# Performance work log

Hardware: AMD Instinct MI355X
Metric: run time of the kernel (lower is better)

## Reference

```python
import jax, jax.numpy as jnp
import numpy as np

TEMPERATURE = 0.6
TOP_K = 50
TOP_P = 0.9
REP_PENALTY = 1.2
BATCH, VOCAB, HIST = 256, 128000, 200


def setup_inputs() -> dict:
    key = jax.random.key(0)
    k1, k2 = jax.random.split(key)
    logits = jax.random.normal(k1, (BATCH, VOCAB), dtype=jnp.float32)
    prev_tokens = jax.random.randint(k2, (BATCH, HIST), 0, VOCAB)
    return {"logits": logits, "prev_tokens": prev_tokens}


def reference(logits, prev_tokens):
    B = logits.shape[0]
    rows = jnp.arange(B)[:, None]  # [B,1] row index for scatter

    # --- repetition penalty: mult if <0 else div, on previously seen tokens ---
    vals = jnp.take_along_axis(logits, prev_tokens, axis=1)  # [B,H]
    penalized = jnp.where(vals < 0, vals * REP_PENALTY, vals / REP_PENALTY)
    logits = logits.at[rows, prev_tokens].set(penalized)

    # --- temperature ---
    logits = logits / TEMPERATURE

    # --- top-k filter: mask everything below the k-th largest logit ---
    kth = jax.lax.top_k(logits, TOP_K)[0][:, -1:]  # [B,1]
    logits = jnp.where(logits < kth, -jnp.inf, logits)

    # --- top-p (nucleus) filter: sort desc, cumsum probs, keep prefix <= p ---
    order = jnp.argsort(-logits, axis=-1)                      # [B,V] desc order
    sorted_logits = jnp.take_along_axis(logits, order, axis=-1)
    cum_probs = jnp.cumsum(jax.nn.softmax(sorted_logits, axis=-1), axis=-1)
    remove_sorted = cum_probs > TOP_P
    # shift right so the first token exceeding p is kept (HF semantics)
    remove_sorted = jnp.concatenate(
        [jnp.zeros_like(remove_sorted[:, :1]), remove_sorted[:, :-1]], axis=-1)
    # scatter mask back to vocab order
    remove = jnp.zeros_like(remove_sorted).at[rows, order].set(remove_sorted)
    logits = jnp.where(remove, -jnp.inf, logits)

    # --- distribution parameter of Multinomial(total_count=compare_sample) ---
    probs = jax.nn.softmax(logits, axis=-1)
    return probs
```

## Files before the change

### kernel.cpp

```cpp
#include <hip/hip_runtime.h>
#include <stdint.h>

#define BATCH    256
#define VOCAB    128000
#define HIST     200
#define TOPK     50
#define CAP      2048
#define NTHREADS 1024
#define BITWORDS (VOCAB / 32)

__device__ __forceinline__ unsigned fkey_of(float f) {
  unsigned u = __float_as_uint(f);
  return (u & 0x80000000u) ? ~u : (u | 0x80000000u);
}
__device__ __forceinline__ float f_of_key(unsigned k) {
  unsigned u = (k & 0x80000000u) ? (k & 0x7FFFFFFFu) : ~k;
  return __uint_as_float(u);
}

__global__ __launch_bounds__(NTHREADS) void sample_head_kernel(
    const float* __restrict__ logits, const int* __restrict__ prev,
    float* __restrict__ out)
{
  __shared__ unsigned bitmask[BITWORDS];
  __shared__ unsigned long long keys[CAP];
  __shared__ float evals[CAP];
  __shared__ int s_count;
  __shared__ int s_m, s_j;
  __shared__ float s_maxx, s_Z2;

  const int b   = blockIdx.x;
  const int tid = threadIdx.x;
  const float* row  = logits + (size_t)b * VOCAB;
  float*       orow = out    + (size_t)b * VOCAB;

  for (int i = tid; i < BITWORDS; i += NTHREADS) bitmask[i] = 0u;
  __syncthreads();
  for (int i = tid; i < HIST; i += NTHREADS) {
    int t = prev[b * HIST + i];
    atomicOr(&bitmask[t >> 5], 1u << (t & 31));
  }
  __syncthreads();

  float T = 3.0f;
  float Tlo = 0.f, Thi = 0.f;
  bool hasLo = false, hasHi = false;
  int cnt = 0;

  const float4* row4  = (const float4*)row;
  float4*       orow4 = (float4*)orow;
  const int N4 = VOCAB / 4;

  for (int attempt = 0; attempt < 40; ++attempt) {
    __syncthreads();
    if (tid == 0) s_count = 0;
    __syncthreads();

    for (int i = tid; i < N4; i += NTHREADS) {
      float4 v4 = row4[i];
      if (attempt == 0) orow4[i] = make_float4(0.f, 0.f, 0.f, 0.f);
      int v0 = i * 4;
      unsigned w  = bitmask[v0 >> 5];
      unsigned sh = v0 & 31;
      float vv[4] = {v4.x, v4.y, v4.z, v4.w};
      #pragma unroll
      for (int l = 0; l < 4; ++l) {
        float v = vv[l];
        float y = v;
        if ((w >> (sh + l)) & 1u)
          y = (v < 0.0f) ? v * 1.2f : v / 1.2f;
        if (y > T) {
          float x = y / 0.6f;
          int pos = atomicAdd(&s_count, 1);
          if (pos < CAP) {
            unsigned k = fkey_of(x);
            keys[pos] = ((unsigned long long)k << 32) |
                        (unsigned)(~(unsigned)(v0 + l));
          }
        }
      }
    }
    __syncthreads();
    cnt = s_count;
    if (cnt >= TOPK && cnt <= CAP) break;
    if (cnt < TOPK) { Thi = T; hasHi = true; T = hasLo ? 0.5f * (T + Tlo) : T - 1.0f; }
    else            { Tlo = T; hasLo = true; T = hasHi ? 0.5f * (T + Thi) : T + 1.0f; }
  }
  if (cnt > CAP) cnt = CAP;

  int n = 64;
  while (n < cnt) n <<= 1;
  for (int i = cnt + tid; i < n; i += NTHREADS) keys[i] = 0ull;
  __syncthreads();
  for (int k = 2; k <= n; k <<= 1) {
    for (int j = k >> 1; j > 0; j >>= 1) {
      for (int i = tid; i < n; i += NTHREADS) {
        int l = i ^ j;
        if (l > i) {
          unsigned long long a = keys[i], c = keys[l];
          bool up = (i & k) == 0;
          if (up ? (a < c) : (a > c)) { keys[i] = c; keys[l] = a; }
        }
      }
      __syncthreads();
    }
  }

  if (tid == 0) {
    int kk = (cnt < TOPK) ? cnt : TOPK;
    unsigned kth = (unsigned)(keys[kk - 1] >> 32);
    int m = kk;
    while (m < cnt && (unsigned)(keys[m] >> 32) == kth) m++;
    s_m = m;
    s_maxx = f_of_key((unsigned)(keys[0] >> 32));
  }
  __syncthreads();
  int m = s_m;
  float maxx = s_maxx;
  for (int i = tid; i < m; i += NTHREADS)
    evals[i] = expf(f_of_key((unsigned)(keys[i] >> 32)) - maxx);
  __syncthreads();

  if (tid == 0) {
    float Z = 0.f;
    for (int i = 0; i < m; ++i) Z += evals[i];
    float cum = 0.f;
    int j = 0;
    for (int i = 0; i < m; ++i) {
      if (i > 0 && cum > 0.9f) break;
      cum += evals[i] / Z;
      j = i + 1;
    }
    float Z2 = 0.f;
    for (int i = 0; i < j; ++i) Z2 += evals[i];
    s_j = j; s_Z2 = Z2;
  }
  __syncthreads();

  int j = s_j;
  float Z2 = s_Z2;
  for (int i = tid; i < j; i += NTHREADS) {
    int idx = (int)(~(unsigned)(keys[i] & 0xFFFFFFFFull));
    orow[idx] = evals[i] / Z2;
  }
}

extern "C" void kernel_launch(void* const* d_in, const int* in_sizes, int n_in,
                              void* d_out, int out_size, void* d_ws, size_t ws_size,
                              hipStream_t stream) {
  const float* logits = (const float*)d_in[0];
  const int*   prev   = (const int*)d_in[1];
  float*       out    = (float*)d_out;
  hipLaunchKernelGGL(sample_head_kernel, dim3(BATCH), dim3(NTHREADS), 0, stream,
                     logits, prev, out);
}
```

Measured before the change: 249.1 us.

## Split into multi-block streaming collect kernel and per-row select kernel

New measurement: 258.1 us. +3.6%, slower.

```diff
diff --git a/kernel.cpp b/kernel.cpp
--- a/kernel.cpp
+++ b/kernel.cpp
@@ -5,9 +5,18 @@
 #define VOCAB    128000
 #define HIST     200
 #define TOPK     50
+#define BITWORDS (VOCAB / 32)
+
+#define SLICES   8
+#define NT1      256
+#define NT2      256
+#define LCAP     1024
+#define TRAW     3.0f
+
 #define CAP      2048
 #define NTHREADS 1024
-#define BITWORDS (VOCAB / 32)
+
+typedef float f32x4_t __attribute__((ext_vector_type(4)));
 
 __device__ __forceinline__ unsigned fkey_of(float f) {
   unsigned u = __float_as_uint(f);
@@ -16,6 +25,172 @@
 __device__ __forceinline__ float f_of_key(unsigned k) {
   unsigned u = (k & 0x80000000u) ? (k & 0x7FFFFFFFu) : ~k;
   return __uint_as_float(u);
+}
+
+__global__ __launch_bounds__(NT1) void stream_collect_kernel(
+    const float* __restrict__ logits, float* __restrict__ out,
+    int* __restrict__ cnt_g, uint2* __restrict__ cand_g)
+{
+  const int bid = blockIdx.x;
+  const int b = bid >> 3;
+  const int s = bid & (SLICES - 1);
+  const float4* row4  = (const float4*)(logits + (size_t)b * VOCAB);
+  float4*       orow4 = (float4*)(out + (size_t)b * VOCAB);
+  const int per = (VOCAB / 4) / SLICES;
+  const int lo = s * per, hi = lo + per;
+  int*   cnt  = cnt_g + b;
+  uint2* cand = cand_g + (size_t)b * LCAP;
+
+  const f32x4_t z4 = (f32x4_t)0.f;
+  for (int i = lo + threadIdx.x; i < hi; i += NT1) {
+    float4 v = row4[i];
+    __builtin_nontemporal_store(z4, (f32x4_t*)&orow4[i]);
+    unsigned v0 = 4u * (unsigned)i;
+    if (v.x > TRAW) { int p = atomicAdd(cnt, 1); if (p < LCAP) cand[p] = make_uint2(__float_as_uint(v.x), v0 + 0u); }
+    if (v.y > TRAW) { int p = atomicAdd(cnt, 1); if (p < LCAP) cand[p] = make_uint2(__float_as_uint(v.y), v0 + 1u); }
+    if (v.z > TRAW) { int p = atomicAdd(cnt, 1); if (p < LCAP) cand[p] = make_uint2(__float_as_uint(v.z), v0 + 2u); }
+    if (v.w > TRAW) { int p = atomicAdd(cnt, 1); if (p < LCAP) cand[p] = make_uint2(__float_as_uint(v.w), v0 + 3u); }
+  }
+}
+
+__global__ __launch_bounds__(NT2) void select_kernel(
+    const float* __restrict__ logits, const int* __restrict__ prev,
+    float* __restrict__ out, const int* __restrict__ cnt_g,
+    const uint2* __restrict__ cand_g)
+{
+  __shared__ unsigned bitmask[BITWORDS];
+  __shared__ unsigned long long keys[LCAP];
+  __shared__ float evals[LCAP];
+  __shared__ int s_cnt, s_good, s_m, s_j;
+  __shared__ float s_maxx, s_Z2;
+
+  const int b   = blockIdx.x;
+  const int tid = threadIdx.x;
+  const float* row  = logits + (size_t)b * VOCAB;
+  float*       orow = out    + (size_t)b * VOCAB;
+
+  for (int i = tid; i < BITWORDS; i += NT2) bitmask[i] = 0u;
+  if (tid == 0) s_good = 0;
+  __syncthreads();
+  for (int i = tid; i < HIST; i += NT2) {
+    int t = prev[b * HIST + i];
+    atomicOr(&bitmask[t >> 5], 1u << (t & 31));
+  }
+  __syncthreads();
+
+  int cnt = cnt_g[b];
+  int mn = cnt < LCAP ? cnt : LCAP;
+  const uint2* cand = cand_g + (size_t)b * LCAP;
+  for (int i = tid; i < mn; i += NT2) {
+    uint2 c = cand[i];
+    float v = __uint_as_float(c.x);
+    unsigned idx = c.y;
+    float y = v;
+    if ((bitmask[idx >> 5] >> (idx & 31)) & 1u)
+      y = (v < 0.0f) ? v * 1.2f : v / 1.2f;
+    float x = y / 0.6f;
+    keys[i] = ((unsigned long long)fkey_of(x) << 32) |
+              (unsigned)(~idx);
+    if (y > TRAW) atomicAdd(&s_good, 1);
+  }
+  __syncthreads();
+
+  if (cnt > LCAP || s_good < TOPK) {
+    float T = TRAW;
+    float Tlo = 0.f, Thi = 0.f;
+    bool hasLo = false, hasHi = false;
+    const float4* row4 = (const float4*)row;
+    const int N4 = VOCAB / 4;
+    for (int attempt = 0; attempt < 40; ++attempt) {
+      __syncthreads();
+      if (tid == 0) s_cnt = 0;
+      __syncthreads();
+      for (int i = tid; i < N4; i += NT2) {
+        float4 v4 = row4[i];
+        int v0 = i * 4;
+        unsigned w  = bitmask[v0 >> 5];
+        unsigned sh = v0 & 31;
+        float vv[4] = {v4.x, v4.y, v4.z, v4.w};
+        #pragma unroll
+        for (int l = 0; l < 4; ++l) {
+          float v = vv[l];
+          float y = v;
+          if ((w >> (sh + l)) & 1u)
+            y = (v < 0.0f) ? v * 1.2f : v / 1.2f;
+          if (y > T) {
+            int pos = atomicAdd(&s_cnt, 1);
+            if (pos < LCAP) {
+              unsigned k = fkey_of(y / 0.6f);
+              keys[pos] = ((unsigned long long)k << 32) |
+                          (unsigned)(~(unsigned)(v0 + l));
+            }
+          }
+        }
+      }
+      __syncthreads();
+      cnt = s_cnt;
+      if (cnt >= TOPK && cnt <= LCAP) break;
+      if (cnt < TOPK) { Thi = T; hasHi = true; T = hasLo ? 0.5f * (T + Tlo) : T - 1.0f; }
+      else            { Tlo = T; hasLo = true; T = hasHi ? 0.5f * (T + Thi) : T + 1.0f; }
+    }
+    if (cnt > LCAP) cnt = LCAP;
+  }
+
+  int n = 64;
+  while (n < cnt) n <<= 1;
+  for (int i = cnt + tid; i < n; i += NT2) keys[i] = 0ull;
+  __syncthreads();
+  for (int k = 2; k <= n; k <<= 1) {
+    for (int j = k >> 1; j > 0; j >>= 1) {
+      for (int i = tid; i < n; i += NT2) {
+        int l = i ^ j;
+        if (l > i) {
+          unsigned long long a = keys[i], c = keys[l];
+          bool up = (i & k) == 0;
+          if (up ? (a < c) : (a > c)) { keys[i] = c; keys[l] = a; }
+        }
+      }
+      __syncthreads();
+    }
+  }
+
+  if (tid == 0) {
+    int kk = (cnt < TOPK) ? cnt : TOPK;
+    unsigned kth = (unsigned)(keys[kk - 1] >> 32);
+    int m = kk;
+    while (m < cnt && (unsigned)(keys[m] >> 32) == kth) m++;
+    s_m = m;
+    s_maxx = f_of_key((unsigned)(keys[0] >> 32));
+  }
+  __syncthreads();
+  int m = s_m;
+  float maxx = s_maxx;
+  for (int i = tid; i < m; i += NT2)
+    evals[i] = expf(f_of_key((unsigned)(keys[i] >> 32)) - maxx);
+  __syncthreads();
+
+  if (tid == 0) {
+    float Z = 0.f;
+    for (int i = 0; i < m; ++i) Z += evals[i];
+    float cum = 0.f;
+    int j = 0;
+    for (int i = 0; i < m; ++i) {
+      if (i > 0 && cum > 0.9f) break;
+      cum += evals[i] / Z;
+      j = i + 1;
+    }
+    float Z2 = 0.f;
+    for (int i = 0; i < j; ++i) Z2 += evals[i];
+    s_j = j; s_Z2 = Z2;
+  }
+  __syncthreads();
+
+  int j = s_j;
+  float Z2 = s_Z2;
+  for (int i = tid; i < j; i += NT2) {
+    int idx = (int)(~(unsigned)(keys[i] & 0xFFFFFFFFull));
+    orow[idx] = evals[i] / Z2;
+  }
 }
 
 __global__ __launch_bounds__(NTHREADS) void sample_head_kernel(
@@ -151,6 +326,21 @@
   const float* logits = (const float*)d_in[0];
   const int*   prev   = (const int*)d_in[1];
   float*       out    = (float*)d_out;
-  hipLaunchKernelGGL(sample_head_kernel, dim3(BATCH), dim3(NTHREADS), 0, stream,
-                     logits, prev, out);
-}
+
+  const size_t cnt_bytes  = (size_t)BATCH * sizeof(int);
+  const size_t cand_off   = 1024;
+  const size_t need       = cand_off + (size_t)BATCH * LCAP * sizeof(uint2);
+
+  if (d_ws != nullptr && ws_size >= need) {
+    int*   cnt_g  = (int*)d_ws;
+    uint2* cand_g = (uint2*)((char*)d_ws + cand_off);
+    hipMemsetAsync(d_ws, 0, cnt_bytes, stream);
+    hipLaunchKernelGGL(stream_collect_kernel, dim3(BATCH * SLICES), dim3(NT1),
+                       0, stream, logits, out, cnt_g, cand_g);
+    hipLaunchKernelGGL(select_kernel, dim3(BATCH), dim3(NT2),
+                       0, stream, logits, prev, out, cnt_g, cand_g);
+  } else {
+    hipLaunchKernelGGL(sample_head_kernel, dim3(BATCH), dim3(NTHREADS),
+                       0, stream, logits, prev, out);
+  }
+}
```
